# Performance work log

Hardware: AMD Instinct MI355X
Metric: run time of the kernel (lower is better)

## Reference

```python
import jax, jax.numpy as jnp
import numpy as np


def setup_inputs() -> dict:
    key = jax.random.key(0)
    k1, k2, k3, k4, k5 = jax.random.split(key, 5)
    N, C, A = 4096, 64, 256
    fc_weight = jax.random.normal(k1, (C, A), dtype=jnp.float32) * 0.05
    features = jax.random.normal(k2, (N, A), dtype=jnp.float32)
    pred = jax.random.normal(k3, (N, C), dtype=jnp.float32)
    labels = jax.random.randint(k4, (N,), 0, C, dtype=jnp.int64)
    # make covariance PSD-ish and small-scale like class-conditional feature covariances
    B = jax.random.normal(k5, (C, A, A), dtype=jnp.float32) * 0.05
    covariance_sample = jnp.einsum('cij,ckj->cik', B, B)  # [C, A, A]
    Lambda = jnp.float32(0.5)
    return {
        'fc_weight': fc_weight,
        'features': features,
        'pred': pred,
        'labels': labels,
        'Lambda': Lambda,
        'covariance_sample': covariance_sample,
    }


def reference(fc_weight, features, pred, labels, Lambda, covariance_sample):
    # fc_weight: [C, A]; pred: [N, C]; labels: [N]; covariance_sample: [C, A, A]
    # ISDA-style augmentation: sigma2[n, c] = (w_c - w_{y_n})^T CV[y_n] (w_c - w_{y_n})
    # torch code builds N×C×C bmm and extracts diagonal; here we compute the
    # quadratic-form diagonal directly (same math, no redundant C× compute).
    labels = labels.astype(jnp.int32)
    diff = fc_weight[None, :, :] - fc_weight[labels][:, None, :]   # [N, C, A]
    cv = covariance_sample[labels]                                  # [N, A, A]
    tmp = jnp.einsum('nca,nab->ncb', diff, cv)                      # [N, C, A]
    sigma2 = Lambda * jnp.einsum('ncb,ncb->nc', tmp, diff)          # [N, C]
    aug_y = pred + 0.5 * sigma2
    # mean cross-entropy (nn.CrossEntropyLoss default reduction='mean')
    logp = jax.nn.log_softmax(aug_y, axis=-1)
    nll = -jnp.take_along_axis(logp, labels[:, None], axis=1)[:, 0]
    return jnp.mean(nll)
```

## Files before the change

### kernel.cpp

```cpp
#include <hip/hip_runtime.h>

#define N_ROWS 4096
#define C_CLS  64
#define A_DIM  256
#define BK     32
#define KCHUNK (A_DIM / BK)
#define LOSS_BLOCKS 256

__global__ __launch_bounds__(256) void qform_kernel(
    const float* __restrict__ W,
    const float* __restrict__ CV,
    float* __restrict__ Spart)
{
    __shared__ float Vt[BK][A_DIM];
    __shared__ float Dt[BK][C_CLS];
    __shared__ float Psum[32][C_CLS];

    const int t  = threadIdx.x;
    const int y  = blockIdx.x >> 3;
    const int kc = blockIdx.x & 7;
    const int kb = kc * BK;

    {
        const float4* src = (const float4*)(CV + ((size_t)y * A_DIM * A_DIM
                                                  + (size_t)kb * A_DIM));
        float4* vdst = (float4*)&Vt[0][0];
        #pragma unroll
        for (int i = 0; i < (BK * A_DIM / 4) / 256; ++i)
            vdst[t + i * 256] = src[t + i * 256];
    }

    {
        const int kq    = (t & 7) * 4;
        const int chalf = t >> 3;
        const float4 wy = *(const float4*)(W + y * A_DIM + kb + kq);
        #pragma unroll
        for (int cc = 0; cc < 2; ++cc) {
            const int c = chalf + cc * 32;
            const float4 wc = *(const float4*)(W + c * A_DIM + kb + kq);
            Dt[kq + 0][c] = wc.x - wy.x;
            Dt[kq + 1][c] = wc.y - wy.y;
            Dt[kq + 2][c] = wc.z - wy.z;
            Dt[kq + 3][c] = wc.w - wy.w;
        }
    }
    __syncthreads();

    const int c0 = (t & 7) * 8;
    const int a0 = (t >> 3) * 8;
    float acc[8][8];
    #pragma unroll
    for (int i = 0; i < 8; ++i)
        #pragma unroll
        for (int j = 0; j < 8; ++j) acc[i][j] = 0.0f;

    #pragma unroll 2
    for (int k = 0; k < BK; ++k) {
        const float4 a_lo = *(const float4*)&Vt[k][a0];
        const float4 a_hi = *(const float4*)&Vt[k][a0 + 4];
        const float4 d_lo = *(const float4*)&Dt[k][c0];
        const float4 d_hi = *(const float4*)&Dt[k][c0 + 4];
        const float af[8] = {a_lo.x, a_lo.y, a_lo.z, a_lo.w,
                             a_hi.x, a_hi.y, a_hi.z, a_hi.w};
        const float df[8] = {d_lo.x, d_lo.y, d_lo.z, d_lo.w,
                             d_hi.x, d_hi.y, d_hi.z, d_hi.w};
        #pragma unroll
        for (int i = 0; i < 8; ++i)
            #pragma unroll
            for (int j = 0; j < 8; ++j)
                acc[i][j] += df[i] * af[j];
    }

    float s[8];
    {
        const float4 wy_lo = *(const float4*)(W + y * A_DIM + a0);
        const float4 wy_hi = *(const float4*)(W + y * A_DIM + a0 + 4);
        const float wyv[8] = {wy_lo.x, wy_lo.y, wy_lo.z, wy_lo.w,
                              wy_hi.x, wy_hi.y, wy_hi.z, wy_hi.w};
        #pragma unroll
        for (int i = 0; i < 8; ++i) {
            const int c = c0 + i;
            const float4 wc_lo = *(const float4*)(W + c * A_DIM + a0);
            const float4 wc_hi = *(const float4*)(W + c * A_DIM + a0 + 4);
            const float wcv[8] = {wc_lo.x, wc_lo.y, wc_lo.z, wc_lo.w,
                                  wc_hi.x, wc_hi.y, wc_hi.z, wc_hi.w};
            float ss = 0.0f;
            #pragma unroll
            for (int j = 0; j < 8; ++j)
                ss += acc[i][j] * (wcv[j] - wyv[j]);
            s[i] = ss;
        }
    }
    const int ag = t >> 3;
    *(float4*)&Psum[ag][c0]     = make_float4(s[0], s[1], s[2], s[3]);
    *(float4*)&Psum[ag][c0 + 4] = make_float4(s[4], s[5], s[6], s[7]);
    __syncthreads();

    if (t < C_CLS) {
        float r = 0.0f;
        #pragma unroll
        for (int g = 0; g < 32; ++g) r += Psum[g][t];
        Spart[(size_t)kc * C_CLS * C_CLS + y * C_CLS + t] = r;
    }
}

__global__ __launch_bounds__(256) void loss_kernel(
    const float* __restrict__ pred,
    const int*   __restrict__ labels,
    const float* __restrict__ lambda_p,
    const float* __restrict__ Spart,
    float* __restrict__ partials)
{
    __shared__ float wsum[4];
    const int t    = threadIdx.x;
    const int lane = t & 63;
    const int wgid = blockIdx.x * 4 + (t >> 6);
    const float lam = 0.5f * lambda_p[0];

    float acc_nll = 0.0f;
    #pragma unroll
    for (int r = 0; r < 4; ++r) {
        const int n = r * 1024 + wgid;
        const int y = labels[n];
        float sp = 0.0f;
        #pragma unroll
        for (int k = 0; k < KCHUNK; ++k)
            sp += Spart[(size_t)k * C_CLS * C_CLS + y * C_CLS + lane];
        const float logit = pred[n * C_CLS + lane] + lam * sp;

        float m = logit;
        #pragma unroll
        for (int off = 32; off > 0; off >>= 1)
            m = fmaxf(m, __shfl_xor(m, off, 64));
        float e = __expf(logit - m);
        float ssum = e;
        #pragma unroll
        for (int off = 32; off > 0; off >>= 1)
            ssum += __shfl_xor(ssum, off, 64);
        const float ly = __shfl(logit, y, 64);
        acc_nll += logf(ssum) + m - ly;
    }

    if (lane == 0) wsum[t >> 6] = acc_nll;
    __syncthreads();
    if (t == 0)
        partials[blockIdx.x] = wsum[0] + wsum[1] + wsum[2] + wsum[3];
}

__global__ __launch_bounds__(256) void finalize_kernel(
    const float* __restrict__ partials, float* __restrict__ out)
{
    __shared__ float wsum[4];
    const int t = threadIdx.x;
    float v = partials[t];
    #pragma unroll
    for (int off = 32; off > 0; off >>= 1)
        v += __shfl_xor(v, off, 64);
    if ((t & 63) == 0) wsum[t >> 6] = v;
    __syncthreads();
    if (t == 0)
        out[0] = (wsum[0] + wsum[1] + wsum[2] + wsum[3]) * (1.0f / (float)N_ROWS);
}

extern "C" void kernel_launch(void* const* d_in, const int* in_sizes, int n_in,
                              void* d_out, int out_size, void* d_ws, size_t ws_size,
                              hipStream_t stream) {
    (void)in_sizes; (void)n_in; (void)out_size; (void)ws_size;
    const float* W      = (const float*)d_in[0];
    const float* pred   = (const float*)d_in[2];
    const int*   labels = (const int*)d_in[3];
    const float* lam    = (const float*)d_in[4];
    const float* CV     = (const float*)d_in[5];
    float* out = (float*)d_out;

    float* Spart    = (float*)d_ws;
    float* partials = (float*)d_ws + KCHUNK * C_CLS * C_CLS;

    qform_kernel<<<dim3(C_CLS * KCHUNK), dim3(256), 0, stream>>>(W, CV, Spart);
    loss_kernel<<<dim3(LOSS_BLOCKS), dim3(256), 0, stream>>>(pred, labels, lam, Spart, partials);
    finalize_kernel<<<dim3(1), dim3(256), 0, stream>>>(partials, out);
}
```

Measured before the change: 88.83 us.

## Fuse quadratic-form, loss and finalize kernels via grid barrier

Merges the three kernel launches into one persistent kernel of 512 blocks. A monotonic atomic grid barrier separates the quadratic-form stage from the loss stage, and a ticket counter picks the last block to do the final reduction. Intermediates move to device globals, which removes two launch gaps and the separate finalize pass. The barrier relies on all 512 blocks being co-resident; launch_bounds(256,2) is added with that in mind, and the design deadlocks if the blocks cannot all fit.

```diff
diff --git a/kernel.cpp b/kernel.cpp
--- a/kernel.cpp
+++ b/kernel.cpp
@@ -5,167 +5,192 @@
 #define A_DIM  256
 #define BK     32
 #define KCHUNK (A_DIM / BK)
-#define LOSS_BLOCKS 256
-
-__global__ __launch_bounds__(256) void qform_kernel(
+#define GRID   (C_CLS * KCHUNK)
+
+__device__ float    g_Spart[KCHUNK * C_CLS * C_CLS];
+__device__ float    g_part[GRID];
+__device__ unsigned g_bar  = 0;
+__device__ unsigned g_tick = 0;
+
+__global__ __launch_bounds__(256, 2) void fused_kernel(
     const float* __restrict__ W,
     const float* __restrict__ CV,
-    float* __restrict__ Spart)
+    const float* __restrict__ pred,
+    const int*   __restrict__ labels,
+    const float* __restrict__ lambda_p,
+    float* __restrict__ out)
 {
     __shared__ float Vt[BK][A_DIM];
     __shared__ float Dt[BK][C_CLS];
     __shared__ float Psum[32][C_CLS];
-
-    const int t  = threadIdx.x;
-    const int y  = blockIdx.x >> 3;
-    const int kc = blockIdx.x & 7;
-    const int kb = kc * BK;
+    __shared__ float wsum4[4];
+    __shared__ int   s_last;
+
+    const int t = threadIdx.x;
 
     {
-        const float4* src = (const float4*)(CV + ((size_t)y * A_DIM * A_DIM
-                                                  + (size_t)kb * A_DIM));
-        float4* vdst = (float4*)&Vt[0][0];
+        const int y  = blockIdx.x >> 3;
+        const int kc = blockIdx.x & 7;
+        const int kb = kc * BK;
+
+        {
+            const float4* src = (const float4*)(CV + ((size_t)y * A_DIM * A_DIM
+                                                      + (size_t)kb * A_DIM));
+            float4* vdst = (float4*)&Vt[0][0];
+            #pragma unroll
+            for (int i = 0; i < (BK * A_DIM / 4) / 256; ++i)
+                vdst[t + i * 256] = src[t + i * 256];
+        }
+
+        {
+            const int kq    = (t & 7) * 4;
+            const int chalf = t >> 3;
+            const float4 wy = *(const float4*)(W + y * A_DIM + kb + kq);
+            #pragma unroll
+            for (int cc = 0; cc < 2; ++cc) {
+                const int c = chalf + cc * 32;
+                const float4 wc = *(const float4*)(W + c * A_DIM + kb + kq);
+                Dt[kq + 0][c] = wc.x - wy.x;
+                Dt[kq + 1][c] = wc.y - wy.y;
+                Dt[kq + 2][c] = wc.z - wy.z;
+                Dt[kq + 3][c] = wc.w - wy.w;
+            }
+        }
+        __syncthreads();
+
+        const int c0 = (t & 7) * 8;
+        const int a0 = (t >> 3) * 8;
+        float acc[8][8];
         #pragma unroll
-        for (int i = 0; i < (BK * A_DIM / 4) / 256; ++i)
-            vdst[t + i * 256] = src[t + i * 256];
+        for (int i = 0; i < 8; ++i)
+            #pragma unroll
+            for (int j = 0; j < 8; ++j) acc[i][j] = 0.0f;
+
+        #pragma unroll 2
+        for (int k = 0; k < BK; ++k) {
+            const float4 a_lo = *(const float4*)&Vt[k][a0];
+            const float4 a_hi = *(const float4*)&Vt[k][a0 + 4];
+            const float4 d_lo = *(const float4*)&Dt[k][c0];
+            const float4 d_hi = *(const float4*)&Dt[k][c0 + 4];
+            const float af[8] = {a_lo.x, a_lo.y, a_lo.z, a_lo.w,
+                                 a_hi.x, a_hi.y, a_hi.z, a_hi.w};
+            const float df[8] = {d_lo.x, d_lo.y, d_lo.z, d_lo.w,
+                                 d_hi.x, d_hi.y, d_hi.z, d_hi.w};
+            #pragma unroll
+            for (int i = 0; i < 8; ++i)
+                #pragma unroll
+                for (int j = 0; j < 8; ++j)
+                    acc[i][j] += df[i] * af[j];
+        }
+
+        float s[8];
+        {
+            const float4 wy_lo = *(const float4*)(W + y * A_DIM + a0);
+            const float4 wy_hi = *(const float4*)(W + y * A_DIM + a0 + 4);
+            const float wyv[8] = {wy_lo.x, wy_lo.y, wy_lo.z, wy_lo.w,
+                                  wy_hi.x, wy_hi.y, wy_hi.z, wy_hi.w};
+            #pragma unroll
+            for (int i = 0; i < 8; ++i) {
+                const int c = c0 + i;
+                const float4 wc_lo = *(const float4*)(W + c * A_DIM + a0);
+                const float4 wc_hi = *(const float4*)(W + c * A_DIM + a0 + 4);
+                const float wcv[8] = {wc_lo.x, wc_lo.y, wc_lo.z, wc_lo.w,
+                                      wc_hi.x, wc_hi.y, wc_hi.z, wc_hi.w};
+                float ss = 0.0f;
+                #pragma unroll
+                for (int j = 0; j < 8; ++j)
+                    ss += acc[i][j] * (wcv[j] - wyv[j]);
+                s[i] = ss;
+            }
+        }
+        const int ag = t >> 3;
+        *(float4*)&Psum[ag][c0]     = make_float4(s[0], s[1], s[2], s[3]);
+        *(float4*)&Psum[ag][c0 + 4] = make_float4(s[4], s[5], s[6], s[7]);
+        __syncthreads();
+
+        if (t < C_CLS) {
+            float r = 0.0f;
+            #pragma unroll
+            for (int g = 0; g < 32; ++g) r += Psum[g][t];
+            g_Spart[(size_t)kc * C_CLS * C_CLS + y * C_CLS + t] = r;
+        }
     }
 
-    {
-        const int kq    = (t & 7) * 4;
-        const int chalf = t >> 3;
-        const float4 wy = *(const float4*)(W + y * A_DIM + kb + kq);
-        #pragma unroll
-        for (int cc = 0; cc < 2; ++cc) {
-            const int c = chalf + cc * 32;
-            const float4 wc = *(const float4*)(W + c * A_DIM + kb + kq);
-            Dt[kq + 0][c] = wc.x - wy.x;
-            Dt[kq + 1][c] = wc.y - wy.y;
-            Dt[kq + 2][c] = wc.z - wy.z;
-            Dt[kq + 3][c] = wc.w - wy.w;
-        }
+    __syncthreads();
+    if (t == 0) {
+        __threadfence();
+        unsigned v = __hip_atomic_fetch_add(&g_bar, 1u, __ATOMIC_ACQ_REL,
+                                            __HIP_MEMORY_SCOPE_AGENT) + 1u;
+        const unsigned target = (v + (GRID - 1u)) & ~(unsigned)(GRID - 1u);
+        while (__hip_atomic_load(&g_bar, __ATOMIC_RELAXED,
+                                 __HIP_MEMORY_SCOPE_AGENT) < target)
+            __builtin_amdgcn_s_sleep(4);
+        __threadfence();
     }
     __syncthreads();
 
-    const int c0 = (t & 7) * 8;
-    const int a0 = (t >> 3) * 8;
-    float acc[8][8];
-    #pragma unroll
-    for (int i = 0; i < 8; ++i)
+    {
+        const int lane = t & 63;
+        const int wv   = t >> 6;
+        const int gw   = (int)blockIdx.x * 4 + wv;
+        const float lam = 0.5f * lambda_p[0];
+
+        float acc_nll = 0.0f;
         #pragma unroll
-        for (int j = 0; j < 8; ++j) acc[i][j] = 0.0f;
-
-    #pragma unroll 2
-    for (int k = 0; k < BK; ++k) {
-        const float4 a_lo = *(const float4*)&Vt[k][a0];
-        const float4 a_hi = *(const float4*)&Vt[k][a0 + 4];
-        const float4 d_lo = *(const float4*)&Dt[k][c0];
-        const float4 d_hi = *(const float4*)&Dt[k][c0 + 4];
-        const float af[8] = {a_lo.x, a_lo.y, a_lo.z, a_lo.w,
-                             a_hi.x, a_hi.y, a_hi.z, a_hi.w};
-        const float df[8] = {d_lo.x, d_lo.y, d_lo.z, d_lo.w,
-                             d_hi.x, d_hi.y, d_hi.z, d_hi.w};
-        #pragma unroll
-        for (int i = 0; i < 8; ++i)
-            #pragma unroll
-            for (int j = 0; j < 8; ++j)
-                acc[i][j] += df[i] * af[j];
+        for (int r = 0; r < 2; ++r) {
+            const int n = r * 2048 + gw;
+            const int y = labels[n];
+            float sp = 0.0f;
+            #pragma unroll
+            for (int k = 0; k < KCHUNK; ++k)
+                sp += g_Spart[k * C_CLS * C_CLS + y * C_CLS + lane];
+            const float logit = pred[n * C_CLS + lane] + lam * sp;
+
+            float m = logit;
+            #pragma unroll
+            for (int off = 32; off > 0; off >>= 1)
+                m = fmaxf(m, __shfl_xor(m, off, 64));
+            float e = __expf(logit - m);
+            float ssum = e;
+            #pragma unroll
+            for (int off = 32; off > 0; off >>= 1)
+                ssum += __shfl_xor(ssum, off, 64);
+            const float ly = __shfl(logit, y, 64);
+            acc_nll += logf(ssum) + m - ly;
+        }
+
+        if (lane == 0) wsum4[wv] = acc_nll;
+        __syncthreads();
+        if (t == 0) {
+            g_part[blockIdx.x] = wsum4[0] + wsum4[1] + wsum4[2] + wsum4[3];
+            __threadfence();
+            unsigned v = __hip_atomic_fetch_add(&g_tick, 1u, __ATOMIC_ACQ_REL,
+                                                __HIP_MEMORY_SCOPE_AGENT) + 1u;
+            s_last = ((v & (GRID - 1u)) == 0u) ? 1 : 0;
+        }
+        __syncthreads();
+
+        if (s_last) {
+            float v = __hip_atomic_load(&g_part[t], __ATOMIC_RELAXED,
+                                        __HIP_MEMORY_SCOPE_AGENT)
+                    + __hip_atomic_load(&g_part[t + 256], __ATOMIC_RELAXED,
+                                        __HIP_MEMORY_SCOPE_AGENT);
+            #pragma unroll
+            for (int off = 32; off > 0; off >>= 1)
+                v += __shfl_xor(v, off, 64);
+            if (lane == 0) wsum4[wv] = v;
+            __syncthreads();
+            if (t == 0)
+                out[0] = (wsum4[0] + wsum4[1] + wsum4[2] + wsum4[3])
+                         * (1.0f / (float)N_ROWS);
+        }
     }
-
-    float s[8];
-    {
-        const float4 wy_lo = *(const float4*)(W + y * A_DIM + a0);
-        const float4 wy_hi = *(const float4*)(W + y * A_DIM + a0 + 4);
-        const float wyv[8] = {wy_lo.x, wy_lo.y, wy_lo.z, wy_lo.w,
-                              wy_hi.x, wy_hi.y, wy_hi.z, wy_hi.w};
-        #pragma unroll
-        for (int i = 0; i < 8; ++i) {
-            const int c = c0 + i;
-            const float4 wc_lo = *(const float4*)(W + c * A_DIM + a0);
-            const float4 wc_hi = *(const float4*)(W + c * A_DIM + a0 + 4);
-            const float wcv[8] = {wc_lo.x, wc_lo.y, wc_lo.z, wc_lo.w,
-                                  wc_hi.x, wc_hi.y, wc_hi.z, wc_hi.w};
-            float ss = 0.0f;
-            #pragma unroll
-            for (int j = 0; j < 8; ++j)
-                ss += acc[i][j] * (wcv[j] - wyv[j]);
-            s[i] = ss;
-        }
-    }
-    const int ag = t >> 3;
-    *(float4*)&Psum[ag][c0]     = make_float4(s[0], s[1], s[2], s[3]);
-    *(float4*)&Psum[ag][c0 + 4] = make_float4(s[4], s[5], s[6], s[7]);
-    __syncthreads();
-
-    if (t < C_CLS) {
-        float r = 0.0f;
-        #pragma unroll
-        for (int g = 0; g < 32; ++g) r += Psum[g][t];
-        Spart[(size_t)kc * C_CLS * C_CLS + y * C_CLS + t] = r;
-    }
-}
-
-__global__ __launch_bounds__(256) void loss_kernel(
-    const float* __restrict__ pred,
-    const int*   __restrict__ labels,
-    const float* __restrict__ lambda_p,
-    const float* __restrict__ Spart,
-    float* __restrict__ partials)
-{
-    __shared__ float wsum[4];
-    const int t    = threadIdx.x;
-    const int lane = t & 63;
-    const int wgid = blockIdx.x * 4 + (t >> 6);
-    const float lam = 0.5f * lambda_p[0];
-
-    float acc_nll = 0.0f;
-    #pragma unroll
-    for (int r = 0; r < 4; ++r) {
-        const int n = r * 1024 + wgid;
-        const int y = labels[n];
-        float sp = 0.0f;
-        #pragma unroll
-        for (int k = 0; k < KCHUNK; ++k)
-            sp += Spart[(size_t)k * C_CLS * C_CLS + y * C_CLS + lane];
-        const float logit = pred[n * C_CLS + lane] + lam * sp;
-
-        float m = logit;
-        #pragma unroll
-        for (int off = 32; off > 0; off >>= 1)
-            m = fmaxf(m, __shfl_xor(m, off, 64));
-        float e = __expf(logit - m);
-        float ssum = e;
-        #pragma unroll
-        for (int off = 32; off > 0; off >>= 1)
-            ssum += __shfl_xor(ssum, off, 64);
-        const float ly = __shfl(logit, y, 64);
-        acc_nll += logf(ssum) + m - ly;
-    }
-
-    if (lane == 0) wsum[t >> 6] = acc_nll;
-    __syncthreads();
-    if (t == 0)
-        partials[blockIdx.x] = wsum[0] + wsum[1] + wsum[2] + wsum[3];
-}
-
-__global__ __launch_bounds__(256) void finalize_kernel(
-    const float* __restrict__ partials, float* __restrict__ out)
-{
-    __shared__ float wsum[4];
-    const int t = threadIdx.x;
-    float v = partials[t];
-    #pragma unroll
-    for (int off = 32; off > 0; off >>= 1)
-        v += __shfl_xor(v, off, 64);
-    if ((t & 63) == 0) wsum[t >> 6] = v;
-    __syncthreads();
-    if (t == 0)
-        out[0] = (wsum[0] + wsum[1] + wsum[2] + wsum[3]) * (1.0f / (float)N_ROWS);
 }
 
 extern "C" void kernel_launch(void* const* d_in, const int* in_sizes, int n_in,
                               void* d_out, int out_size, void* d_ws, size_t ws_size,
                               hipStream_t stream) {
-    (void)in_sizes; (void)n_in; (void)out_size; (void)ws_size;
+    (void)in_sizes; (void)n_in; (void)out_size; (void)d_ws; (void)ws_size;
     const float* W      = (const float*)d_in[0];
     const float* pred   = (const float*)d_in[2];
     const int*   labels = (const int*)d_in[3];
@@ -173,10 +198,5 @@
     const float* CV     = (const float*)d_in[5];
     float* out = (float*)d_out;
 
-    float* Spart    = (float*)d_ws;
-    float* partials = (float*)d_ws + KCHUNK * C_CLS * C_CLS;
-
-    qform_kernel<<<dim3(C_CLS * KCHUNK), dim3(256), 0, stream>>>(W, CV, Spart);
-    loss_kernel<<<dim3(LOSS_BLOCKS), dim3(256), 0, stream>>>(pred, labels, lam, Spart, partials);
-    finalize_kernel<<<dim3(1), dim3(256), 0, stream>>>(partials, out);
+    fused_kernel<<<dim3(GRID), dim3(256), 0, stream>>>(W, CV, pred, labels, lam, out);
 }
```

Result: slower. 146.5 us (+64.9%).

## Restructure quadratic-form kernel to per-lane class with wave-uniform covariance column tiles

Applied to the files above, without the earlier changes.

The quadratic-form kernel now splits work by output column block instead of by reduction chunk. Each lane owns one class and each wave owns 8 covariance columns, and the loop reads covariance and the label weight row through wave-uniform addresses that can become scalar loads. LDS staging of covariance and the weight differences is gone, and the class weight row is kept in registers with double buffering. This removes the shared-memory traffic and barriers. In exchange, each wave now streams the full 256-row reduction through scalar or broadcast loads with long dependency chains, and each lane holds many more registers.

```diff
diff --git a/kernel.cpp b/kernel.cpp
--- a/kernel.cpp
+++ b/kernel.cpp
@@ -3,104 +3,89 @@
 #define N_ROWS 4096
 #define C_CLS  64
 #define A_DIM  256
-#define BK     32
-#define KCHUNK (A_DIM / BK)
+#define KCHUNK 8
 #define LOSS_BLOCKS 256
+
 
 __global__ __launch_bounds__(256) void qform_kernel(
     const float* __restrict__ W,
     const float* __restrict__ CV,
     float* __restrict__ Spart)
 {
-    __shared__ float Vt[BK][A_DIM];
-    __shared__ float Dt[BK][C_CLS];
-    __shared__ float Psum[32][C_CLS];
+    __shared__ float Psum[4][C_CLS];
 
-    const int t  = threadIdx.x;
-    const int y  = blockIdx.x >> 3;
-    const int kc = blockIdx.x & 7;
-    const int kb = kc * BK;
+    const int t    = threadIdx.x;
+    const int lane = t & 63;
+    const int wv   = __builtin_amdgcn_readfirstlane(t >> 6);
+    const int y    = blockIdx.x >> 3;
+    const int ab   = blockIdx.x & 7;
+    const int a0   = ab * 32 + wv * 8;
 
-    {
-        const float4* src = (const float4*)(CV + ((size_t)y * A_DIM * A_DIM
-                                                  + (size_t)kb * A_DIM));
-        float4* vdst = (float4*)&Vt[0][0];
-        #pragma unroll
-        for (int i = 0; i < (BK * A_DIM / 4) / 256; ++i)
-            vdst[t + i * 256] = src[t + i * 256];
+    const float* __restrict__ cvp = CV + (size_t)y * A_DIM * A_DIM + a0;
+    const float* __restrict__ wyp = W + y * A_DIM;
+    const float* __restrict__ wcp = W + lane * A_DIM;
+
+    float acc[8];
+    #pragma unroll
+    for (int j = 0; j < 8; ++j) acc[j] = 0.0f;
+
+    float cur[32], nxt[32];
+    #pragma unroll
+    for (int i = 0; i < 8; ++i) {
+        const float4 v = ((const float4*)wcp)[i];
+        cur[4*i+0] = v.x; cur[4*i+1] = v.y; cur[4*i+2] = v.z; cur[4*i+3] = v.w;
     }
 
-    {
-        const int kq    = (t & 7) * 4;
-        const int chalf = t >> 3;
-        const float4 wy = *(const float4*)(W + y * A_DIM + kb + kq);
+    #pragma unroll 1
+    for (int pc = 0; pc < 4; ++pc) {
+        const int b0 = pc * 64;
+
         #pragma unroll
-        for (int cc = 0; cc < 2; ++cc) {
-            const int c = chalf + cc * 32;
-            const float4 wc = *(const float4*)(W + c * A_DIM + kb + kq);
-            Dt[kq + 0][c] = wc.x - wy.x;
-            Dt[kq + 1][c] = wc.y - wy.y;
-            Dt[kq + 2][c] = wc.z - wy.z;
-            Dt[kq + 3][c] = wc.w - wy.w;
+        for (int i = 0; i < 8; ++i) {
+            const float4 v = ((const float4*)wcp)[(2*pc+1)*8 + i];
+            nxt[4*i+0] = v.x; nxt[4*i+1] = v.y; nxt[4*i+2] = v.z; nxt[4*i+3] = v.w;
+        }
+        #pragma unroll
+        for (int bi = 0; bi < 32; ++bi) {
+            const int b = b0 + bi;
+            const float d = cur[bi] - wyp[b];
+            #pragma unroll
+            for (int j = 0; j < 8; ++j)
+                acc[j] = fmaf(d, cvp[(size_t)b * A_DIM + j], acc[j]);
+        }
+
+        const int nc = (2*pc + 2 < 8) ? (2*pc + 2) : 7;
+        #pragma unroll
+        for (int i = 0; i < 8; ++i) {
+            const float4 v = ((const float4*)wcp)[nc*8 + i];
+            cur[4*i+0] = v.x; cur[4*i+1] = v.y; cur[4*i+2] = v.z; cur[4*i+3] = v.w;
+        }
+        #pragma unroll
+        for (int bi = 0; bi < 32; ++bi) {
+            const int b = b0 + 32 + bi;
+            const float d = nxt[bi] - wyp[b];
+            #pragma unroll
+            for (int j = 0; j < 8; ++j)
+                acc[j] = fmaf(d, cvp[(size_t)b * A_DIM + j], acc[j]);
         }
     }
-    __syncthreads();
 
-    const int c0 = (t & 7) * 8;
-    const int a0 = (t >> 3) * 8;
-    float acc[8][8];
-    #pragma unroll
-    for (int i = 0; i < 8; ++i)
+    float s = 0.0f;
+    {
+        const float4 wa_lo = *(const float4*)(wcp + a0);
+        const float4 wa_hi = *(const float4*)(wcp + a0 + 4);
+        const float wav[8] = {wa_lo.x, wa_lo.y, wa_lo.z, wa_lo.w,
+                              wa_hi.x, wa_hi.y, wa_hi.z, wa_hi.w};
         #pragma unroll
-        for (int j = 0; j < 8; ++j) acc[i][j] = 0.0f;
-
-    #pragma unroll 2
-    for (int k = 0; k < BK; ++k) {
-        const float4 a_lo = *(const float4*)&Vt[k][a0];
-        const float4 a_hi = *(const float4*)&Vt[k][a0 + 4];
-        const float4 d_lo = *(const float4*)&Dt[k][c0];
-        const float4 d_hi = *(const float4*)&Dt[k][c0 + 4];
-        const float af[8] = {a_lo.x, a_lo.y, a_lo.z, a_lo.w,
-                             a_hi.x, a_hi.y, a_hi.z, a_hi.w};
-        const float df[8] = {d_lo.x, d_lo.y, d_lo.z, d_lo.w,
-                             d_hi.x, d_hi.y, d_hi.z, d_hi.w};
-        #pragma unroll
-        for (int i = 0; i < 8; ++i)
-            #pragma unroll
-            for (int j = 0; j < 8; ++j)
-                acc[i][j] += df[i] * af[j];
+        for (int j = 0; j < 8; ++j)
+            s = fmaf(acc[j], wav[j] - wyp[a0 + j], s);
     }
-
-    float s[8];
-    {
-        const float4 wy_lo = *(const float4*)(W + y * A_DIM + a0);
-        const float4 wy_hi = *(const float4*)(W + y * A_DIM + a0 + 4);
-        const float wyv[8] = {wy_lo.x, wy_lo.y, wy_lo.z, wy_lo.w,
-                              wy_hi.x, wy_hi.y, wy_hi.z, wy_hi.w};
-        #pragma unroll
-        for (int i = 0; i < 8; ++i) {
-            const int c = c0 + i;
-            const float4 wc_lo = *(const float4*)(W + c * A_DIM + a0);
-            const float4 wc_hi = *(const float4*)(W + c * A_DIM + a0 + 4);
-            const float wcv[8] = {wc_lo.x, wc_lo.y, wc_lo.z, wc_lo.w,
-                                  wc_hi.x, wc_hi.y, wc_hi.z, wc_hi.w};
-            float ss = 0.0f;
-            #pragma unroll
-            for (int j = 0; j < 8; ++j)
-                ss += acc[i][j] * (wcv[j] - wyv[j]);
-            s[i] = ss;
-        }
-    }
-    const int ag = t >> 3;
-    *(float4*)&Psum[ag][c0]     = make_float4(s[0], s[1], s[2], s[3]);
-    *(float4*)&Psum[ag][c0 + 4] = make_float4(s[4], s[5], s[6], s[7]);
+    Psum[wv][lane] = s;
     __syncthreads();
 
     if (t < C_CLS) {
-        float r = 0.0f;
-        #pragma unroll
-        for (int g = 0; g < 32; ++g) r += Psum[g][t];
-        Spart[(size_t)kc * C_CLS * C_CLS + y * C_CLS + t] = r;
+        const float r = Psum[0][t] + Psum[1][t] + Psum[2][t] + Psum[3][t];
+        Spart[(size_t)ab * C_CLS * C_CLS + y * C_CLS + t] = r;
     }
 }
 
```

Measured after the change: 131.6 us. +48.2%, slower.
